# Performance work log

Hardware: AMD Instinct MI355X
Metric: run time of the kernel (lower is better)

Reference implementation:

```python
import jax, jax.numpy as jnp
import numpy as np
from jax import lax

B, T, I, H, L, C = 128, 784, 1, 256, 20, 10  # batch, seq_len, input, hidden, layers, classes


def setup_inputs() -> dict:
    key = jax.random.key(0)
    ks = jax.random.split(key, 9)
    s = 1.0 / np.sqrt(H)  # torch nn.RNN init: U(-1/sqrt(H), 1/sqrt(H))
    u = lambda k, shape: jax.random.uniform(k, shape, jnp.float32, -s, s)
    return {
        "x": jax.random.normal(ks[0], (B, T, I), jnp.float32),
        "W_ih0": u(ks[1], (H, I)),        # layer 0 input proj
        "b_ih0": u(ks[2], (H,)),
        "W_ih": u(ks[3], (L - 1, H, H)),  # layers 1..L-1 input proj
        "b_ih": u(ks[4], (L - 1, H)),
        "W_hh": u(ks[5], (L, H, H)),      # recurrent weights, all layers
        "b_hh": u(ks[6], (L, H)),
        "W_fc": u(ks[7], (C, H)),         # classification head
        "b_fc": u(ks[8], (C,)),
    }


def _rnn_layer(x_seq, W_ih, b_ih, W_hh, b_hh):
    """One vanilla relu-RNN layer. x_seq: [B,T,in] -> [B,T,H]."""
    # Hoist the input projection out of the scan (batched GEMM over all timesteps).
    xp = jnp.einsum('bti,hi->bth', x_seq, W_ih) + b_ih  # [B,T,H]
    h0 = jnp.zeros((x_seq.shape[0], W_hh.shape[0]), x_seq.dtype)

    def step(h, xt):
        h = jax.nn.relu(xt + h @ W_hh.T + b_hh)
        return h, h

    _, ys = lax.scan(step, h0, jnp.swapaxes(xp, 0, 1))  # scan over time
    return jnp.swapaxes(ys, 0, 1)  # [B,T,H]


def reference(x, W_ih0, b_ih0, W_ih, b_ih, W_hh, b_hh, W_fc, b_fc):
    h = _rnn_layer(x, W_ih0, b_ih0, W_hh[0], b_hh[0])
    for l in range(L - 1):  # fixed small layer loop
        h = _rnn_layer(h, W_ih[l], b_ih[l], W_hh[l + 1], b_hh[l + 1])
    last_hidden = h[:, -1, :]  # [B,H]
    return last_hidden @ W_fc.T + b_fc  # [B,C]
```

## Files before the change

kernel.cpp:

```cpp
#include <hip/hip_runtime.h>
#include <hip/hip_fp16.h>


#define B_    128
#define T_    784
#define H_    256
#define L_    20
#define C_    10
#define G_    8
#define BM_   16
#define S_    4
#define NS_   196
#define SW_   280
#define RQWS_ 4096
#define TPB_  512

typedef _Float16 v8h __attribute__((ext_vector_type(8)));
typedef _Float16 v4h __attribute__((ext_vector_type(4)));
typedef float    v4f __attribute__((ext_vector_type(4)));
typedef unsigned long long u64;

__global__ __launch_bounds__(TPB_, 1)
void rnn_wavefront(const float* __restrict__ x,
                   const float* __restrict__ W_ih0,
                   const float* __restrict__ b_ih0,
                   const float* __restrict__ W_ih,
                   const float* __restrict__ b_ih,
                   const float* __restrict__ W_hh,
                   const float* __restrict__ b_hh,
                   const float* __restrict__ W_fc,
                   const float* __restrict__ b_fc,
                   float* __restrict__ out,
                   unsigned* __restrict__ prod,
                   unsigned* __restrict__ cons,
                   u64* __restrict__ ring,
                   int rmask)
{
    const int l    = blockIdx.x >> 3;
    const int g    = blockIdx.x & 7;
    const int tid  = threadIdx.x;
    const int lane = tid & 63;
    const int wave = tid >> 6;
    const int quad = lane >> 4;
    const int s16  = lane & 15;
    const int nbase = wave * 32;
    const int m_e  = tid >> 5;
    const int n_e  = (tid & 31) * 8;

    __shared__ __align__(16) _Float16 bufX[S_][BM_][SW_];
    __shared__ __align__(16) _Float16 lH[2][BM_][SW_];

    for (int i = tid; i < 2 * BM_ * SW_; i += TPB_) (&lH[0][0][0])[i] = (_Float16)0.f;

    v8h wf[16][2];
#pragma unroll
    for (int kt = 0; kt < 16; ++kt) {
        const int k0 = kt * 32 + quad * 8;
#pragma unroll
        for (int nt = 0; nt < 2; ++nt) {
            const int j = nbase + nt * 16 + s16;
            v8h w;
            if (kt < 8) {
                if (l == 0) {
#pragma unroll
                    for (int i = 0; i < 8; ++i) w[i] = (_Float16)0.f;
                } else {
                    const float* src = &W_ih[(((size_t)(l - 1) * H_) + j) * H_ + k0];
#pragma unroll
                    for (int i = 0; i < 8; ++i) w[i] = (_Float16)src[i];
                }
            } else {
                const float* src = &W_hh[(((size_t)l * H_) + j) * H_ + (k0 - 256)];
#pragma unroll
                for (int i = 0; i < 8; ++i) w[i] = (_Float16)src[i];
            }
            wf[kt][nt] = w;
        }
    }

    float bias[2], w0v[2];
#pragma unroll
    for (int nt = 0; nt < 2; ++nt) {
        const int j = nbase + nt * 16 + s16;
        bias[nt] = b_hh[l * H_ + j] + ((l == 0) ? b_ih0[j] : b_ih[(l - 1) * H_ + j]);
        w0v[nt]  = (l == 0) ? W_ih0[j] : 0.f;
    }

    unsigned* upprod = prod + ((l > 0 ? l - 1 : 0) * G_ + g);
    unsigned* myprod = prod + (l * G_ + g);
    unsigned* mycons = cons + (l * G_ + g);
    unsigned* dncons = cons + (((l < L_ - 1) ? l + 1 : l) * G_ + g);
    const unsigned R = (unsigned)rmask + 1u;
    u64* myring = ring + ((size_t)(l * G_ + g) * (size_t)R) * RQWS_;
    u64* upring = ring + ((size_t)((l > 0 ? l - 1 : 0) * G_ + g) * (size_t)R) * RQWS_;

    unsigned pSeen = 0, cSeen = 0;
    const size_t eidx = (size_t)m_e * 64 + (size_t)(tid & 31) * 2;

    if (l > 0) {
        if (tid == 64) {
            while (pSeen < 2u) {
                pSeen = __hip_atomic_load(upprod, __ATOMIC_RELAXED,
                                          __HIP_MEMORY_SCOPE_AGENT);
                if (pSeen < 2u) __builtin_amdgcn_s_sleep(2);
            }
        }
        __syncthreads();
#pragma unroll
        for (int jj = 0; jj < S_; ++jj) {
            u64 v0 = __hip_atomic_load(upring + (size_t)jj * 1024 + eidx,
                                       __ATOMIC_RELAXED, __HIP_MEMORY_SCOPE_AGENT);
            u64 v1 = __hip_atomic_load(upring + (size_t)jj * 1024 + eidx + 1,
                                       __ATOMIC_RELAXED, __HIP_MEMORY_SCOPE_AGENT);
            *(u64*)&bufX[jj][m_e][n_e]     = v0;
            *(u64*)&bufX[jj][m_e][n_e + 4] = v1;
        }
    }

    for (int s = 0; s < NS_; ++s) {
        const bool pfOK = (l > 0) && (s + 1 < NS_);
        u64 pfv[S_][2];
        v4h XPh[S_][2];

#pragma unroll
        for (int j = 0; j < S_; ++j) {
            const int t = S_ * s + j;
            __syncthreads();

            if (j == 0) {
                if (tid == 0 && l > 0)
                    __hip_atomic_store(mycons, (unsigned)(s + 1), __ATOMIC_RELAXED,
                                       __HIP_MEMORY_SCOPE_AGENT);
                if (tid == 64 && pfOK) {
                    const unsigned tgt = (unsigned)(s + 2);
                    while (pSeen < tgt) {
                        pSeen = __hip_atomic_load(upprod, __ATOMIC_RELAXED,
                                                  __HIP_MEMORY_SCOPE_AGENT);
                        if (pSeen < tgt) __builtin_amdgcn_s_sleep(2);
                    }
                }
                if (tid == 128 && l < L_ - 1 && s >= (int)R) {
                    const unsigned tgt = (unsigned)(s - (int)R + 1);
                    while (cSeen < tgt) {
                        cSeen = __hip_atomic_load(dncons, __ATOMIC_RELAXED,
                                                  __HIP_MEMORY_SCOPE_AGENT);
                        if (cSeen < tgt) __builtin_amdgcn_s_sleep(2);
                    }
                }

                if (l > 0) {
                    v4f xpa[S_][2];
#pragma unroll
                    for (int jj = 0; jj < S_; ++jj)
#pragma unroll
                        for (int nt = 0; nt < 2; ++nt)
                            xpa[jj][nt] = (v4f){bias[nt], bias[nt], bias[nt], bias[nt]};
#pragma unroll
                    for (int jj = 0; jj < S_; ++jj) {
#pragma unroll
                        for (int kt = 0; kt < 8; ++kt) {
                            v8h a = *(const v8h*)&bufX[jj][s16][kt * 32 + quad * 8];
                            xpa[jj][0] = __builtin_amdgcn_mfma_f32_16x16x32_f16(a, wf[kt][0], xpa[jj][0], 0, 0, 0);
                            xpa[jj][1] = __builtin_amdgcn_mfma_f32_16x16x32_f16(a, wf[kt][1], xpa[jj][1], 0, 0, 0);
                        }
                    }
#pragma unroll
                    for (int jj = 0; jj < S_; ++jj)
#pragma unroll
                        for (int nt = 0; nt < 2; ++nt)
#pragma unroll
                            for (int r = 0; r < 4; ++r)
                                XPh[jj][nt][r] = (_Float16)xpa[jj][nt][r];
                } else {
#pragma unroll
                    for (int jj = 0; jj < S_; ++jj)
#pragma unroll
                        for (int r = 0; r < 4; ++r) {
                            float xv = x[(size_t)(g * BM_ + quad * 4 + r) * T_ + (S_ * s + jj)];
#pragma unroll
                            for (int nt = 0; nt < 2; ++nt)
                                XPh[jj][nt][r] = (_Float16)(bias[nt] + xv * w0v[nt]);
                        }
                }
            }

            if (j == 1) {
                if (tid == 0 && l < L_ - 1 && s >= 1)
                    __hip_atomic_store(myprod, (unsigned)s, __ATOMIC_RELAXED,
                                       __HIP_MEMORY_SCOPE_AGENT);
                if (pfOK) {
                    const u64* base = upring + (size_t)((s + 1) & rmask) * RQWS_;
#pragma unroll
                    for (int jj = 0; jj < S_; ++jj) {
                        pfv[jj][0] = __hip_atomic_load(base + (size_t)jj * 1024 + eidx,
                                                       __ATOMIC_RELAXED,
                                                       __HIP_MEMORY_SCOPE_AGENT);
                        pfv[jj][1] = __hip_atomic_load(base + (size_t)jj * 1024 + eidx + 1,
                                                       __ATOMIC_RELAXED,
                                                       __HIP_MEMORY_SCOPE_AGENT);
                    }
                }
            }

            if (l < L_ - 1 && t > 0) {
                u64 e0 = *(const u64*)&lH[t & 1][m_e][n_e];
                u64 e1 = *(const u64*)&lH[t & 1][m_e][n_e + 4];
                u64* d = myring + (size_t)(((t - 1) >> 2) & rmask) * RQWS_
                                + (size_t)((t - 1) & 3) * 1024 + eidx;
                __hip_atomic_store(d,     e0, __ATOMIC_RELAXED, __HIP_MEMORY_SCOPE_AGENT);
                __hip_atomic_store(d + 1, e1, __ATOMIC_RELAXED, __HIP_MEMORY_SCOPE_AGENT);
            }

            v4f acc0 = (v4f){0.f, 0.f, 0.f, 0.f};
            v4f acc1 = (v4f){0.f, 0.f, 0.f, 0.f};
#pragma unroll
            for (int kt = 8; kt < 16; ++kt) {
                v8h a = *(const v8h*)&lH[t & 1][s16][(kt - 8) * 32 + quad * 8];
                acc0 = __builtin_amdgcn_mfma_f32_16x16x32_f16(a, wf[kt][0], acc0, 0, 0, 0);
                acc1 = __builtin_amdgcn_mfma_f32_16x16x32_f16(a, wf[kt][1], acc1, 0, 0, 0);
            }

#pragma unroll
            for (int nt = 0; nt < 2; ++nt) {
                const v4f av = nt ? acc1 : acc0;
                const int n = nbase + nt * 16 + s16;
#pragma unroll
                for (int r = 0; r < 4; ++r) {
                    float v = (float)XPh[j][nt][r] + av[r];
                    v = fmaxf(v, 0.f);
                    lH[(t + 1) & 1][quad * 4 + r][n] = (_Float16)v;
                }
            }

            if (j == S_ - 1) {
                __syncthreads();
                if (pfOK) {
#pragma unroll
                    for (int jj = 0; jj < S_; ++jj) {
                        *(u64*)&bufX[jj][m_e][n_e]     = pfv[jj][0];
                        *(u64*)&bufX[jj][m_e][n_e + 4] = pfv[jj][1];
                    }
                }
            }
        }
    }

    if (l < L_ - 1) {
        u64 e0 = *(const u64*)&lH[0][m_e][n_e];
        u64 e1 = *(const u64*)&lH[0][m_e][n_e + 4];
        u64* d = myring + (size_t)(((T_ - 1) >> 2) & rmask) * RQWS_
                        + (size_t)3 * 1024 + eidx;
        __hip_atomic_store(d,     e0, __ATOMIC_RELAXED, __HIP_MEMORY_SCOPE_AGENT);
        __hip_atomic_store(d + 1, e1, __ATOMIC_RELAXED, __HIP_MEMORY_SCOPE_AGENT);
        __syncthreads();
        if (tid == 0)
            __hip_atomic_store(myprod, (unsigned)NS_, __ATOMIC_RELAXED,
                               __HIP_MEMORY_SCOPE_AGENT);
    } else {
        __syncthreads();
        if (tid < BM_ * C_) {
            const int bl = tid / C_;
            const int c  = tid % C_;
            float sum = b_fc[c];
            for (int k = 0; k < H_; ++k) sum += (float)lH[0][bl][k] * W_fc[c * H_ + k];
            out[(size_t)(g * BM_ + bl) * C_ + c] = sum;
        }
    }
}

extern "C" void kernel_launch(void* const* d_in, const int* in_sizes, int n_in,
                              void* d_out, int out_size, void* d_ws, size_t ws_size,
                              hipStream_t stream) {
    const float* x     = (const float*)d_in[0];
    const float* W_ih0 = (const float*)d_in[1];
    const float* b_ih0 = (const float*)d_in[2];
    const float* W_ih  = (const float*)d_in[3];
    const float* b_ih  = (const float*)d_in[4];
    const float* W_hh  = (const float*)d_in[5];
    const float* b_hh  = (const float*)d_in[6];
    const float* W_fc  = (const float*)d_in[7];
    const float* b_fc  = (const float*)d_in[8];
    float* out = (float*)d_out;

    const size_t cntBytes = (size_t)L_ * G_ * sizeof(unsigned);
    unsigned* prod = (unsigned*)d_ws;
    unsigned* cons = (unsigned*)((char*)d_ws + cntBytes);
    u64* ring      = (u64*)((char*)d_ws + 2 * cntBytes);

    const size_t slotBytes = (size_t)RQWS_ * 8;
    const size_t base = 2 * cntBytes;
    int R = 4;
    if (ws_size >= base + (size_t)L_ * G_ * 16 * slotBytes) R = 16;
    else if (ws_size >= base + (size_t)L_ * G_ * 8 * slotBytes) R = 8;

    hipMemsetAsync(d_ws, 0, 2 * cntBytes, stream);

    rnn_wavefront<<<dim3(L_ * G_), dim3(TPB_), 0, stream>>>(
        x, W_ih0, b_ih0, W_ih, b_ih, W_hh, b_hh, W_fc, b_fc,
        out, prod, cons, ring, R - 1);
}
```

Before: 1.122 ms.

## Software-pipeline input projection one chunk ahead, interleaved with recurrent steps

Moves the per-chunk input-projection MFMAs off the step-0 critical path. Each timestep now computes one projection for the next chunk after its recurrent update, keeping the current and next projections in double-buffered registers. The prefetch from the upstream ring now runs two chunks ahead, with consumer/producer counters adjusted to match, and the recurrent MFMA is placed before the ring store. Launch bounds change to allow two blocks per CU, which tightens the register budget and risks spills given the extra XP registers.

```diff
diff --git a/kernel.cpp b/kernel.cpp
--- a/kernel.cpp
+++ b/kernel.cpp
@@ -20,7 +20,7 @@
 typedef float    v4f __attribute__((ext_vector_type(4)));
 typedef unsigned long long u64;
 
-__global__ __launch_bounds__(TPB_, 1)
+__global__ __launch_bounds__(TPB_, 2)
 void rnn_wavefront(const float* __restrict__ x,
                    const float* __restrict__ W_ih0,
                    const float* __restrict__ b_ih0,
@@ -97,6 +97,9 @@
     unsigned pSeen = 0, cSeen = 0;
     const size_t eidx = (size_t)m_e * 64 + (size_t)(tid & 31) * 2;
 
+    v4h XPc[S_][2];
+    v4h XPn[S_][2];
+
     if (l > 0) {
         if (tid == 64) {
             while (pSeen < 2u) {
@@ -115,12 +118,47 @@
             *(u64*)&bufX[jj][m_e][n_e]     = v0;
             *(u64*)&bufX[jj][m_e][n_e + 4] = v1;
         }
+        __syncthreads();
+#pragma unroll
+        for (int jj = 0; jj < S_; ++jj) {
+            v4f xp0 = (v4f){bias[0], bias[0], bias[0], bias[0]};
+            v4f xp1 = (v4f){bias[1], bias[1], bias[1], bias[1]};
+#pragma unroll
+            for (int kt = 0; kt < 8; ++kt) {
+                v8h a = *(const v8h*)&bufX[jj][s16][kt * 32 + quad * 8];
+                xp0 = __builtin_amdgcn_mfma_f32_16x16x32_f16(a, wf[kt][0], xp0, 0, 0, 0);
+                xp1 = __builtin_amdgcn_mfma_f32_16x16x32_f16(a, wf[kt][1], xp1, 0, 0, 0);
+            }
+#pragma unroll
+            for (int r = 0; r < 4; ++r) { XPc[jj][0][r] = (_Float16)xp0[r];
+                                          XPc[jj][1][r] = (_Float16)xp1[r]; }
+        }
+        __syncthreads();
+#pragma unroll
+        for (int jj = 0; jj < S_; ++jj) {
+            u64 v0 = __hip_atomic_load(upring + RQWS_ + (size_t)jj * 1024 + eidx,
+                                       __ATOMIC_RELAXED, __HIP_MEMORY_SCOPE_AGENT);
+            u64 v1 = __hip_atomic_load(upring + RQWS_ + (size_t)jj * 1024 + eidx + 1,
+                                       __ATOMIC_RELAXED, __HIP_MEMORY_SCOPE_AGENT);
+            *(u64*)&bufX[jj][m_e][n_e]     = v0;
+            *(u64*)&bufX[jj][m_e][n_e + 4] = v1;
+        }
+    } else {
+#pragma unroll
+        for (int jj = 0; jj < S_; ++jj)
+#pragma unroll
+            for (int r = 0; r < 4; ++r) {
+                float xv = x[(size_t)(g * BM_ + quad * 4 + r) * T_ + jj];
+#pragma unroll
+                for (int nt = 0; nt < 2; ++nt)
+                    XPc[jj][nt][r] = (_Float16)(bias[nt] + xv * w0v[nt]);
+            }
     }
 
     for (int s = 0; s < NS_; ++s) {
-        const bool pfOK = (l > 0) && (s + 1 < NS_);
+        const bool xpnOK = (s + 1 < NS_);
+        const bool pfOK  = (l > 0) && (s + 2 < NS_);
         u64 pfv[S_][2];
-        v4h XPh[S_][2];
 
 #pragma unroll
         for (int j = 0; j < S_; ++j) {
@@ -129,10 +167,10 @@
 
             if (j == 0) {
                 if (tid == 0 && l > 0)
-                    __hip_atomic_store(mycons, (unsigned)(s + 1), __ATOMIC_RELAXED,
+                    __hip_atomic_store(mycons, (unsigned)(s + 2), __ATOMIC_RELAXED,
                                        __HIP_MEMORY_SCOPE_AGENT);
                 if (tid == 64 && pfOK) {
-                    const unsigned tgt = (unsigned)(s + 2);
+                    const unsigned tgt = (unsigned)(s + 3);
                     while (pSeen < tgt) {
                         pSeen = __hip_atomic_load(upprod, __ATOMIC_RELAXED,
                                                   __HIP_MEMORY_SCOPE_AGENT);
@@ -147,41 +185,6 @@
                         if (cSeen < tgt) __builtin_amdgcn_s_sleep(2);
                     }
                 }
-
-                if (l > 0) {
-                    v4f xpa[S_][2];
-#pragma unroll
-                    for (int jj = 0; jj < S_; ++jj)
-#pragma unroll
-                        for (int nt = 0; nt < 2; ++nt)
-                            xpa[jj][nt] = (v4f){bias[nt], bias[nt], bias[nt], bias[nt]};
-#pragma unroll
-                    for (int jj = 0; jj < S_; ++jj) {
-#pragma unroll
-                        for (int kt = 0; kt < 8; ++kt) {
-                            v8h a = *(const v8h*)&bufX[jj][s16][kt * 32 + quad * 8];
-                            xpa[jj][0] = __builtin_amdgcn_mfma_f32_16x16x32_f16(a, wf[kt][0], xpa[jj][0], 0, 0, 0);
-                            xpa[jj][1] = __builtin_amdgcn_mfma_f32_16x16x32_f16(a, wf[kt][1], xpa[jj][1], 0, 0, 0);
-                        }
-                    }
-#pragma unroll
-                    for (int jj = 0; jj < S_; ++jj)
-#pragma unroll
-                        for (int nt = 0; nt < 2; ++nt)
-#pragma unroll
-                            for (int r = 0; r < 4; ++r)
-                                XPh[jj][nt][r] = (_Float16)xpa[jj][nt][r];
-                } else {
-#pragma unroll
-                    for (int jj = 0; jj < S_; ++jj)
-#pragma unroll
-                        for (int r = 0; r < 4; ++r) {
-                            float xv = x[(size_t)(g * BM_ + quad * 4 + r) * T_ + (S_ * s + jj)];
-#pragma unroll
-                            for (int nt = 0; nt < 2; ++nt)
-                                XPh[jj][nt][r] = (_Float16)(bias[nt] + xv * w0v[nt]);
-                        }
-                }
             }
 
             if (j == 1) {
@@ -189,7 +192,7 @@
                     __hip_atomic_store(myprod, (unsigned)s, __ATOMIC_RELAXED,
                                        __HIP_MEMORY_SCOPE_AGENT);
                 if (pfOK) {
-                    const u64* base = upring + (size_t)((s + 1) & rmask) * RQWS_;
+                    const u64* base = upring + (size_t)((s + 2) & rmask) * RQWS_;
 #pragma unroll
                     for (int jj = 0; jj < S_; ++jj) {
                         pfv[jj][0] = __hip_atomic_load(base + (size_t)jj * 1024 + eidx,
@@ -202,6 +205,15 @@
                 }
             }
 
+            v4f acc0 = (v4f){0.f, 0.f, 0.f, 0.f};
+            v4f acc1 = (v4f){0.f, 0.f, 0.f, 0.f};
+#pragma unroll
+            for (int kt = 8; kt < 16; ++kt) {
+                v8h a = *(const v8h*)&lH[t & 1][s16][(kt - 8) * 32 + quad * 8];
+                acc0 = __builtin_amdgcn_mfma_f32_16x16x32_f16(a, wf[kt][0], acc0, 0, 0, 0);
+                acc1 = __builtin_amdgcn_mfma_f32_16x16x32_f16(a, wf[kt][1], acc1, 0, 0, 0);
+            }
+
             if (l < L_ - 1 && t > 0) {
                 u64 e0 = *(const u64*)&lH[t & 1][m_e][n_e];
                 u64 e1 = *(const u64*)&lH[t & 1][m_e][n_e + 4];
@@ -211,24 +223,39 @@
                 __hip_atomic_store(d + 1, e1, __ATOMIC_RELAXED, __HIP_MEMORY_SCOPE_AGENT);
             }
 
-            v4f acc0 = (v4f){0.f, 0.f, 0.f, 0.f};
-            v4f acc1 = (v4f){0.f, 0.f, 0.f, 0.f};
-#pragma unroll
-            for (int kt = 8; kt < 16; ++kt) {
-                v8h a = *(const v8h*)&lH[t & 1][s16][(kt - 8) * 32 + quad * 8];
-                acc0 = __builtin_amdgcn_mfma_f32_16x16x32_f16(a, wf[kt][0], acc0, 0, 0, 0);
-                acc1 = __builtin_amdgcn_mfma_f32_16x16x32_f16(a, wf[kt][1], acc1, 0, 0, 0);
-            }
-
 #pragma unroll
             for (int nt = 0; nt < 2; ++nt) {
                 const v4f av = nt ? acc1 : acc0;
                 const int n = nbase + nt * 16 + s16;
 #pragma unroll
                 for (int r = 0; r < 4; ++r) {
-                    float v = (float)XPh[j][nt][r] + av[r];
+                    float v = (float)XPc[j][nt][r] + av[r];
                     v = fmaxf(v, 0.f);
                     lH[(t + 1) & 1][quad * 4 + r][n] = (_Float16)v;
+                }
+            }
+
+            if (xpnOK) {
+                if (l > 0) {
+                    v4f xp0 = (v4f){bias[0], bias[0], bias[0], bias[0]};
+                    v4f xp1 = (v4f){bias[1], bias[1], bias[1], bias[1]};
+#pragma unroll
+                    for (int kt = 0; kt < 8; ++kt) {
+                        v8h a = *(const v8h*)&bufX[j][s16][kt * 32 + quad * 8];
+                        xp0 = __builtin_amdgcn_mfma_f32_16x16x32_f16(a, wf[kt][0], xp0, 0, 0, 0);
+                        xp1 = __builtin_amdgcn_mfma_f32_16x16x32_f16(a, wf[kt][1], xp1, 0, 0, 0);
+                    }
+#pragma unroll
+                    for (int r = 0; r < 4; ++r) { XPn[j][0][r] = (_Float16)xp0[r];
+                                                  XPn[j][1][r] = (_Float16)xp1[r]; }
+                } else {
+#pragma unroll
+                    for (int r = 0; r < 4; ++r) {
+                        float xv = x[(size_t)(g * BM_ + quad * 4 + r) * T_ + (t + S_)];
+#pragma unroll
+                        for (int nt = 0; nt < 2; ++nt)
+                            XPn[j][nt][r] = (_Float16)(bias[nt] + xv * w0v[nt]);
+                    }
                 }
             }
 
@@ -239,6 +266,13 @@
                     for (int jj = 0; jj < S_; ++jj) {
                         *(u64*)&bufX[jj][m_e][n_e]     = pfv[jj][0];
                         *(u64*)&bufX[jj][m_e][n_e + 4] = pfv[jj][1];
+                    }
+                }
+                if (xpnOK) {
+#pragma unroll
+                    for (int jj = 0; jj < S_; ++jj) {
+                        XPc[jj][0] = XPn[jj][0];
+                        XPc[jj][1] = XPn[jj][1];
                     }
                 }
             }
```

Result: slower. 1.179 ms (+5.1%).
